# Kernel tuning notes

Hardware: AMD Instinct MI355X
Metric: run time of the kernel (lower is better)

The kernel has to match this reference:

```python
import jax, jax.numpy as jnp
import numpy as np

N = 8192          # number of nodes
IN_F = 256        # in_features
OUT_F = 128       # out_features
ALPHA = 0.2       # LeakyReLU negative slope


def setup_inputs() -> dict:
    key = jax.random.key(0)
    k1, k2, k3, k4 = jax.random.split(key, 4)
    h = jax.random.normal(k1, (N, IN_F), dtype=jnp.float32)
    adj = jax.random.randint(k2, (N, N), 0, 2, dtype=jnp.int32)  # dense 0/1 adjacency mask
    W = (jax.random.normal(k3, (IN_F, OUT_F), dtype=jnp.float32) * 0.05)   # W.weight^T
    a = (jax.random.normal(k4, (2 * OUT_F,), dtype=jnp.float32) * 0.05)    # a.weight flattened
    return {"h": h, "adj": adj, "W": W, "a": a}


def reference(h, adj, W, a):
    # Wh = self.W(h): [N, OUT_F]
    Wh = h @ W
    # Original builds an [N, N, 2F] concat tensor then projects with 'a'.
    # Equivalent math: e[i, j] = leaky_relu(Wh[i]@a1 + Wh[j]@a2)
    a1, a2 = a[:OUT_F], a[OUT_F:]
    src = Wh @ a1                                     # [N] per-source score
    dst = Wh @ a2                                     # [N] per-target score
    e = jax.nn.leaky_relu(src[:, None] + dst[None, :], negative_slope=ALPHA)  # [N, N]
    # masked softmax over neighbors (dim=1); adj==0 -> -inf
    e = jnp.where(adj == 0, -jnp.inf, e)
    attention = jax.nn.softmax(e, axis=1)             # [N, N]
    # dropout p=0 in eval-mode reference -> identity
    h_prime = attention @ Wh                          # [N, OUT_F]
    return jax.nn.elu(h_prime)                        # concat=True -> ELU
```

## Files before the change

### kernel.cpp

```cpp
#include <hip/hip_runtime.h>
#include <math.h>

#define N 8192
#define IN_F 256
#define OUT_F 128
#define ALPHA 0.2f

typedef _Float16 f16;
typedef __attribute__((ext_vector_type(4))) float f32x4;
typedef __attribute__((ext_vector_type(8))) _Float16 f16x8;
typedef __attribute__((ext_vector_type(4))) _Float16 f16x4;

__global__ __launch_bounds__(256) void k_prep(const float* __restrict__ W,
                                              f16* __restrict__ WT) {
    int idx = blockIdx.x * 256 + threadIdx.x;
    int f = idx >> 8;
    int k = idx & 255;
    WT[idx] = (f16)W[k * OUT_F + f];
}

#define HS 280
__global__ __launch_bounds__(256) void k_wh(const float* __restrict__ h,
                                            const f16* __restrict__ WT,
                                            const float* __restrict__ a,
                                            f16* __restrict__ WhT,
                                            float* __restrict__ src,
                                            float* __restrict__ dst) {
    __shared__ __align__(16) f16 hA[32][HS];
    __shared__ __align__(16) f16 outT[128][40];
    __shared__ float sred[4][32], dred[4][32];

    const int t = threadIdx.x;
    const int i0 = blockIdx.x * 32;
    const int wv = t >> 6, l = t & 63, ln = l & 15, lq = l >> 4;

    {
        const float4* hg = (const float4*)(h + (size_t)i0 * IN_F);
#pragma unroll
        for (int it = 0; it < 8; ++it) {
            int idx = t + it * 256;
            int r = idx >> 6;
            int c4 = (idx & 63) * 4;
            float4 v = hg[idx];
            f16x4 p = { (f16)v.x, (f16)v.y, (f16)v.z, (f16)v.w };
            *(f16x4*)&hA[r][c4] = p;
        }
    }
    __syncthreads();

    f32x4 acc00 = {0.f,0.f,0.f,0.f}, acc01 = {0.f,0.f,0.f,0.f};
    f32x4 acc10 = {0.f,0.f,0.f,0.f}, acc11 = {0.f,0.f,0.f,0.f};
    const int f0 = 32 * wv;

#pragma unroll
    for (int ks = 0; ks < 8; ++ks) {
        const int k0 = 32 * ks + 8 * lq;
        f16x8 a0 = *(const f16x8*)&hA[ln][k0];
        f16x8 a1 = *(const f16x8*)&hA[16 + ln][k0];
        f16x8 b0 = *(const f16x8*)(WT + (size_t)(f0 + ln) * IN_F + k0);
        f16x8 b1 = *(const f16x8*)(WT + (size_t)(f0 + 16 + ln) * IN_F + k0);
        acc00 = __builtin_amdgcn_mfma_f32_16x16x32_f16(a0, b0, acc00, 0, 0, 0);
        acc01 = __builtin_amdgcn_mfma_f32_16x16x32_f16(a0, b1, acc01, 0, 0, 0);
        acc10 = __builtin_amdgcn_mfma_f32_16x16x32_f16(a1, b0, acc10, 0, 0, 0);
        acc11 = __builtin_amdgcn_mfma_f32_16x16x32_f16(a1, b1, acc11, 0, 0, 0);
    }

    const float a1c0 = a[f0 + ln],      a2c0 = a[128 + f0 + ln];
    const float a1c1 = a[f0 + 16 + ln], a2c1 = a[128 + f0 + 16 + ln];
    float sp[8], dp[8];
#pragma unroll
    for (int i = 0; i < 8; ++i) { sp[i] = 0.f; dp[i] = 0.f; }

#pragma unroll
    for (int hh = 0; hh < 2; ++hh) {
        f32x4 v0 = hh ? acc10 : acc00;
        f32x4 v1 = hh ? acc11 : acc01;
        f16x4 p0, p1;
#pragma unroll
        for (int rg = 0; rg < 4; ++rg) {
            sp[hh * 4 + rg] += v0[rg] * a1c0 + v1[rg] * a1c1;
            dp[hh * 4 + rg] += v0[rg] * a2c0 + v1[rg] * a2c1;
            p0[rg] = (f16)v0[rg];
            p1[rg] = (f16)v1[rg];
        }
        *(f16x4*)&outT[f0 + ln][16 * hh + 4 * lq] = p0;
        *(f16x4*)&outT[f0 + 16 + ln][16 * hh + 4 * lq] = p1;
    }
#pragma unroll
    for (int i = 0; i < 8; ++i) {
        float s = sp[i], d = dp[i];
        s += __shfl_down(s, 8, 16); d += __shfl_down(d, 8, 16);
        s += __shfl_down(s, 4, 16); d += __shfl_down(d, 4, 16);
        s += __shfl_down(s, 2, 16); d += __shfl_down(d, 2, 16);
        s += __shfl_down(s, 1, 16); d += __shfl_down(d, 1, 16);
        if (ln == 0) {
            int row = 16 * (i >> 2) + 4 * lq + (i & 3);
            sred[wv][row] = s;
            dred[wv][row] = d;
        }
    }
    __syncthreads();
    if (t < 32) {
        src[i0 + t] = sred[0][t] + sred[1][t] + sred[2][t] + sred[3][t];
        dst[i0 + t] = dred[0][t] + dred[1][t] + dred[2][t] + dred[3][t];
    }
    {
        const int col = t & 127, g = t >> 7;
        const int ct = i0 >> 7, jo = i0 & 127;
        f16x8 q0 = *(const f16x8*)&outT[col][16 * g];
        f16x8 q1 = *(const f16x8*)&outT[col][16 * g + 8];
        f16* dstp = WhT + (size_t)ct * (128 * 128) + (size_t)col * 128 + jo + 16 * g;
        *(f16x8*)(dstp) = q0;
        *(f16x8*)(dstp + 8) = q1;
    }
}

#define TI 16
#define NJ 128
#define JS 2
#define NCL (N / NJ / JS)
#define WSTRIDE 152
__global__ __launch_bounds__(256, 4) void k_attn(const int* __restrict__ adj,
                                                 const f16* __restrict__ WhT,
                                                 const float* __restrict__ src,
                                                 const float* __restrict__ dst,
                                                 float* __restrict__ p_part,
                                                 float* __restrict__ l_part) {
    __shared__ __align__(16) f16 wA[2][TI][WSTRIDE];
    __shared__ float lfin[TI];

    const int t = threadIdx.x;
    const int i0 = blockIdx.x * TI;
    const int jh = blockIdx.y;
    const int pr = t >> 4;
    const int pm = t & 15;
    const int wv = t >> 6;
    const int l = t & 63, ln = l & 15, lq = l >> 4;

    const float my_src = src[i0 + pr];
    const float cshift = fabsf(my_src) + 4.0f;
    float lp = 0.f;
    f32x4 accv0 = {0.f,0.f,0.f,0.f}, accv1 = {0.f,0.f,0.f,0.f};

    const int* arow = adj + (size_t)(i0 + pr) * N + jh * (N / JS) + 8 * pm;
    const float* drow = dst + jh * (N / JS) + 8 * pm;
    const f16* Bb = WhT + (size_t)(jh * NCL) * (128 * 128)
                  + (size_t)(32 * wv + ln) * 128 + 8 * lq;

    int4 aA0, aB0, aA1, aB1;
    float4 dA0, dB0, dA1, dB1;

    auto issue = [&](int c, int4& xA, int4& xB, float4& xdA, float4& xdB) {
        const int j0 = c * NJ;
        xA = *(const int4*)(arow + j0);
        xB = *(const int4*)(arow + j0 + 4);
        xdA = *(const float4*)(drow + j0);
        xdB = *(const float4*)(drow + j0 + 4);
    };
    auto produce = [&](int c, const int4& xA, const int4& xB,
                       const float4& xdA, const float4& xdB) {
        float w[8];
        const int*   av = (const int*)&xA;
        const int*   bv = (const int*)&xB;
        const float* df = (const float*)&xdA;
        const float* ef = (const float*)&xdB;
#pragma unroll
        for (int k = 0; k < 4; ++k) {
            float e = my_src + df[k];
            float lk = e > 0.f ? e : ALPHA * e;
            w[k] = av[k] ? __expf(lk - cshift) : 0.f;
        }
#pragma unroll
        for (int k = 0; k < 4; ++k) {
            float e = my_src + ef[k];
            float lk = e > 0.f ? e : ALPHA * e;
            w[4 + k] = bv[k] ? __expf(lk - cshift) : 0.f;
        }
        f16x8 wp;
#pragma unroll
        for (int k = 0; k < 8; ++k) { lp += w[k]; wp[k] = (f16)w[k]; }
        *(f16x8*)&wA[c & 1][pr][8 * pm] = wp;
    };
    auto mpass = [&](int c) {
        const f16* wb = &wA[c & 1][0][0];
        const f16* bp = Bb + (size_t)c * (128 * 128);
#pragma unroll
        for (int ks = 0; ks < 4; ++ks) {
            const int k0 = 32 * ks;
            f16x8 a0 = *(const f16x8*)(wb + ln * WSTRIDE + k0 + 8 * lq);
            f16x8 b0 = *(const f16x8*)(bp + k0);
            f16x8 b1 = *(const f16x8*)(bp + 16 * 128 + k0);
            accv0 = __builtin_amdgcn_mfma_f32_16x16x32_f16(a0, b0, accv0, 0, 0, 0);
            accv1 = __builtin_amdgcn_mfma_f32_16x16x32_f16(a0, b1, accv1, 0, 0, 0);
        }
    };

    issue(0, aA0, aB0, dA0, dB0);
    produce(0, aA0, aB0, dA0, dB0);
    issue(1, aA1, aB1, dA1, dB1);
    __syncthreads();

    for (int cc = 0; cc < NCL; cc += 2) {
        if (cc + 2 < NCL) issue(cc + 2, aA0, aB0, dA0, dB0);
        mpass(cc);
        produce(cc + 1, aA1, aB1, dA1, dB1);
        __syncthreads();
        if (cc + 3 < NCL) issue(cc + 3, aA1, aB1, dA1, dB1);
        mpass(cc + 1);
        if (cc + 2 < NCL) produce(cc + 2, aA0, aB0, dA0, dB0);
        __syncthreads();
    }

    {
        float v = lp;
        v += __shfl_down(v, 8, 16);
        v += __shfl_down(v, 4, 16);
        v += __shfl_down(v, 2, 16);
        v += __shfl_down(v, 1, 16);
        if (pm == 0) lfin[pr] = v;
    }
    __syncthreads();
    if (t < TI) l_part[(size_t)jh * N + i0 + t] = lfin[t];

    float* pb = p_part + (size_t)jh * N * OUT_F;
#pragma unroll
    for (int hh = 0; hh < 2; ++hh) {
        f32x4 av = hh ? accv1 : accv0;
#pragma unroll
        for (int rg = 0; rg < 4; ++rg) {
            const int row = 4 * lq + rg;
            pb[(size_t)(i0 + row) * OUT_F + 32 * wv + 16 * hh + ln] = av[rg];
        }
    }
}

__global__ __launch_bounds__(256) void k_comb(const float* __restrict__ p_part,
                                              const float* __restrict__ l_part,
                                              float* __restrict__ out) {
    const int idx = blockIdx.x * 256 + threadIdx.x;
    const int row = idx >> 7;
    float p = p_part[idx] + p_part[(size_t)N * OUT_F + idx];
    float lsum = l_part[row] + l_part[N + row];
    float hp = p / lsum;
    out[idx] = hp > 0.f ? hp : expm1f(hp);
}

extern "C" void kernel_launch(void* const* d_in, const int* in_sizes, int n_in,
                              void* d_out, int out_size, void* d_ws, size_t ws_size,
                              hipStream_t stream) {
    const float* h   = (const float*)d_in[0];
    const int*   adj = (const int*)d_in[1];
    const float* W   = (const float*)d_in[2];
    const float* a   = (const float*)d_in[3];
    float* out = (float*)d_out;

    char* ws = (char*)d_ws;
    f16*   WT     = (f16*)ws;                       ws += 64 * 1024;
    f16*   WhT    = (f16*)ws;                       ws += 2 * 1024 * 1024;
    float* src    = (float*)ws;                     ws += N * sizeof(float);
    float* dst    = (float*)ws;                     ws += N * sizeof(float);
    float* l_part = (float*)ws;                     ws += JS * N * sizeof(float);
    float* p_part = (float*)ws;

    k_prep<<<128, 256, 0, stream>>>(W, WT);
    k_wh<<<N / 32, 256, 0, stream>>>(h, WT, a, WhT, src, dst);
    dim3 agrid(N / TI, JS);
    k_attn<<<agrid, 256, 0, stream>>>(adj, WhT, src, dst, p_part, l_part);
    k_comb<<<N * OUT_F / 256, 256, 0, stream>>>(p_part, l_part, out);
}
```

Measured before the change: 450.1 us.

## Restructure attention kernel: per-wave 32-row tiles with register-resident weights, 8-way j split

```diff
diff --git a/kernel.cpp b/kernel.cpp
--- a/kernel.cpp
+++ b/kernel.cpp
@@ -5,6 +5,8 @@
 #define IN_F 256
 #define OUT_F 128
 #define ALPHA 0.2f
+#define JS 8
+#define NSTEP 32
 
 typedef _Float16 f16;
 typedef __attribute__((ext_vector_type(4))) float f32x4;
@@ -115,121 +117,110 @@
     }
 }
 
-#define TI 16
-#define NJ 128
-#define JS 2
-#define NCL (N / NJ / JS)
-#define WSTRIDE 152
-__global__ __launch_bounds__(256, 4) void k_attn(const int* __restrict__ adj,
+__global__ __launch_bounds__(256, 2) void k_attn(const int* __restrict__ adj,
                                                  const f16* __restrict__ WhT,
                                                  const float* __restrict__ src,
                                                  const float* __restrict__ dst,
                                                  float* __restrict__ p_part,
                                                  float* __restrict__ l_part) {
-    __shared__ __align__(16) f16 wA[2][TI][WSTRIDE];
-    __shared__ float lfin[TI];
-
     const int t = threadIdx.x;
-    const int i0 = blockIdx.x * TI;
-    const int jh = blockIdx.y;
-    const int pr = t >> 4;
-    const int pm = t & 15;
-    const int wv = t >> 6;
-    const int l = t & 63, ln = l & 15, lq = l >> 4;
-
-    const float my_src = src[i0 + pr];
-    const float cshift = fabsf(my_src) + 4.0f;
-    float lp = 0.f;
-    f32x4 accv0 = {0.f,0.f,0.f,0.f}, accv1 = {0.f,0.f,0.f,0.f};
-
-    const int* arow = adj + (size_t)(i0 + pr) * N + jh * (N / JS) + 8 * pm;
-    const float* drow = dst + jh * (N / JS) + 8 * pm;
-    const f16* Bb = WhT + (size_t)(jh * NCL) * (128 * 128)
-                  + (size_t)(32 * wv + ln) * 128 + 8 * lq;
-
-    int4 aA0, aB0, aA1, aB1;
-    float4 dA0, dB0, dA1, dB1;
-
-    auto issue = [&](int c, int4& xA, int4& xB, float4& xdA, float4& xdB) {
-        const int j0 = c * NJ;
-        xA = *(const int4*)(arow + j0);
-        xB = *(const int4*)(arow + j0 + 4);
-        xdA = *(const float4*)(drow + j0);
-        xdB = *(const float4*)(drow + j0 + 4);
+    const int wv = t >> 6, l = t & 63, ln = l & 15, lq = l >> 4;
+    const int i0 = (blockIdx.x * 4 + wv) * 32;
+    const int jq = blockIdx.y;
+    const int jbase = jq * (N / JS);
+
+    const float src0 = src[i0 + ln];
+    const float src1 = src[i0 + 16 + ln];
+    const float c0 = fabsf(src0) + 4.0f;
+    const float c1 = fabsf(src1) + 4.0f;
+    float lp0 = 0.f, lp1 = 0.f;
+
+    f32x4 acc0[8], acc1[8];
+#pragma unroll
+    for (int ft = 0; ft < 8; ++ft) {
+        acc0[ft] = (f32x4){0.f,0.f,0.f,0.f};
+        acc1[ft] = (f32x4){0.f,0.f,0.f,0.f};
+    }
+
+    const int* arow0 = adj + (size_t)(i0 + ln) * N + jbase + 8 * lq;
+    const int* arow1 = arow0 + (size_t)16 * N;
+    const float* drow = dst + jbase + 8 * lq;
+    const f16* Bb = WhT + (size_t)(jq * 8) * (128 * 128) + (size_t)ln * 128 + 8 * lq;
+
+    int4 pa0[2][2], pa1[2][2];
+    float4 pd[2][2];
+
+    auto issue = [&](int s, int p) {
+        const int off = 32 * (s & (NSTEP - 1));
+        pa0[p][0] = *(const int4*)(arow0 + off);
+        pa0[p][1] = *(const int4*)(arow0 + off + 4);
+        pa1[p][0] = *(const int4*)(arow1 + off);
+        pa1[p][1] = *(const int4*)(arow1 + off + 4);
+        pd[p][0]  = *(const float4*)(drow + off);
+        pd[p][1]  = *(const float4*)(drow + off + 4);
     };
-    auto produce = [&](int c, const int4& xA, const int4& xB,
-                       const float4& xdA, const float4& xdB) {
-        float w[8];
-        const int*   av = (const int*)&xA;
-        const int*   bv = (const int*)&xB;
-        const float* df = (const float*)&xdA;
-        const float* ef = (const float*)&xdB;
+
+    issue(0, 0);
+    issue(1, 1);
+
+#pragma unroll 4
+    for (int s = 0; s < NSTEP; ++s) {
+        const int p = s & 1;
+        const int4 a00 = pa0[p][0], a01 = pa0[p][1];
+        const int4 a10 = pa1[p][0], a11 = pa1[p][1];
+        const float4 d0 = pd[p][0], d1 = pd[p][1];
+        issue(s + 2, p);
+
+        const int* av0 = (const int*)&a00;
+        const int* av1 = (const int*)&a01;
+        const int* bv0 = (const int*)&a10;
+        const int* bv1 = (const int*)&a11;
+        const float* df0 = (const float*)&d0;
+        const float* df1 = (const float*)&d1;
+
+        f16x8 af0, af1;
 #pragma unroll
         for (int k = 0; k < 4; ++k) {
-            float e = my_src + df[k];
-            float lk = e > 0.f ? e : ALPHA * e;
-            w[k] = av[k] ? __expf(lk - cshift) : 0.f;
+            float e0 = src0 + df0[k];
+            float w0 = av0[k] ? __expf(fmaxf(e0, ALPHA * e0) - c0) : 0.f;
+            lp0 += w0; af0[k] = (f16)w0;
+            float e1 = src1 + df0[k];
+            float w1 = bv0[k] ? __expf(fmaxf(e1, ALPHA * e1) - c1) : 0.f;
+            lp1 += w1; af1[k] = (f16)w1;
         }
 #pragma unroll
         for (int k = 0; k < 4; ++k) {
-            float e = my_src + ef[k];
-            float lk = e > 0.f ? e : ALPHA * e;
-            w[4 + k] = bv[k] ? __expf(lk - cshift) : 0.f;
-        }
-        f16x8 wp;
-#pragma unroll
-        for (int k = 0; k < 8; ++k) { lp += w[k]; wp[k] = (f16)w[k]; }
-        *(f16x8*)&wA[c & 1][pr][8 * pm] = wp;
-    };
-    auto mpass = [&](int c) {
-        const f16* wb = &wA[c & 1][0][0];
-        const f16* bp = Bb + (size_t)c * (128 * 128);
-#pragma unroll
-        for (int ks = 0; ks < 4; ++ks) {
-            const int k0 = 32 * ks;
-            f16x8 a0 = *(const f16x8*)(wb + ln * WSTRIDE + k0 + 8 * lq);
-            f16x8 b0 = *(const f16x8*)(bp + k0);
-            f16x8 b1 = *(const f16x8*)(bp + 16 * 128 + k0);
-            accv0 = __builtin_amdgcn_mfma_f32_16x16x32_f16(a0, b0, accv0, 0, 0, 0);
-            accv1 = __builtin_amdgcn_mfma_f32_16x16x32_f16(a0, b1, accv1, 0, 0, 0);
-        }
-    };
-
-    issue(0, aA0, aB0, dA0, dB0);
-    produce(0, aA0, aB0, dA0, dB0);
-    issue(1, aA1, aB1, dA1, dB1);
-    __syncthreads();
-
-    for (int cc = 0; cc < NCL; cc += 2) {
-        if (cc + 2 < NCL) issue(cc + 2, aA0, aB0, dA0, dB0);
-        mpass(cc);
-        produce(cc + 1, aA1, aB1, dA1, dB1);
-        __syncthreads();
-        if (cc + 3 < NCL) issue(cc + 3, aA1, aB1, dA1, dB1);
-        mpass(cc + 1);
-        if (cc + 2 < NCL) produce(cc + 2, aA0, aB0, dA0, dB0);
-        __syncthreads();
-    }
-
-    {
-        float v = lp;
-        v += __shfl_down(v, 8, 16);
-        v += __shfl_down(v, 4, 16);
-        v += __shfl_down(v, 2, 16);
-        v += __shfl_down(v, 1, 16);
-        if (pm == 0) lfin[pr] = v;
-    }
-    __syncthreads();
-    if (t < TI) l_part[(size_t)jh * N + i0 + t] = lfin[t];
-
-    float* pb = p_part + (size_t)jh * N * OUT_F;
-#pragma unroll
-    for (int hh = 0; hh < 2; ++hh) {
-        f32x4 av = hh ? accv1 : accv0;
+            float e0 = src0 + df1[k];
+            float w0 = av1[k] ? __expf(fmaxf(e0, ALPHA * e0) - c0) : 0.f;
+            lp0 += w0; af0[4 + k] = (f16)w0;
+            float e1 = src1 + df1[k];
+            float w1 = bv1[k] ? __expf(fmaxf(e1, ALPHA * e1) - c1) : 0.f;
+            lp1 += w1; af1[4 + k] = (f16)w1;
+        }
+
+        const f16* bp = Bb + (s >> 2) * (128 * 128) + (s & 3) * 32;
+#pragma unroll
+        for (int ft = 0; ft < 8; ++ft) {
+            f16x8 bf = *(const f16x8*)(bp + ft * (16 * 128));
+            acc0[ft] = __builtin_amdgcn_mfma_f32_16x16x32_f16(af0, bf, acc0[ft], 0, 0, 0);
+            acc1[ft] = __builtin_amdgcn_mfma_f32_16x16x32_f16(af1, bf, acc1[ft], 0, 0, 0);
+        }
+    }
+
+    lp0 += __shfl_down(lp0, 32); lp0 += __shfl_down(lp0, 16);
+    lp1 += __shfl_down(lp1, 32); lp1 += __shfl_down(lp1, 16);
+    if (l < 16) {
+        l_part[(size_t)jq * N + i0 + l] = lp0;
+        l_part[(size_t)jq * N + i0 + 16 + l] = lp1;
+    }
+
+    float* pb = p_part + (size_t)jq * N * OUT_F;
+#pragma unroll
+    for (int ft = 0; ft < 8; ++ft) {
 #pragma unroll
         for (int rg = 0; rg < 4; ++rg) {
-            const int row = 4 * lq + rg;
-            pb[(size_t)(i0 + row) * OUT_F + 32 * wv + 16 * hh + ln] = av[rg];
+            pb[(size_t)(i0 + 4 * lq + rg) * OUT_F + 16 * ft + ln] = acc0[ft][rg];
+            pb[(size_t)(i0 + 16 + 4 * lq + rg) * OUT_F + 16 * ft + ln] = acc1[ft][rg];
         }
     }
 }
@@ -237,12 +228,24 @@
 __global__ __launch_bounds__(256) void k_comb(const float* __restrict__ p_part,
                                               const float* __restrict__ l_part,
                                               float* __restrict__ out) {
-    const int idx = blockIdx.x * 256 + threadIdx.x;
-    const int row = idx >> 7;
-    float p = p_part[idx] + p_part[(size_t)N * OUT_F + idx];
-    float lsum = l_part[row] + l_part[N + row];
-    float hp = p / lsum;
-    out[idx] = hp > 0.f ? hp : expm1f(hp);
+    const int idx4 = blockIdx.x * 256 + threadIdx.x;
+    const int row = idx4 >> 5;
+    const float4* pp = (const float4*)p_part;
+    float4 p = pp[idx4];
+    float lsum = l_part[row];
+#pragma unroll
+    for (int q = 1; q < JS; ++q) {
+        float4 v = pp[(size_t)q * (N * OUT_F / 4) + idx4];
+        p.x += v.x; p.y += v.y; p.z += v.z; p.w += v.w;
+        lsum += l_part[(size_t)q * N + row];
+    }
+    float inv = 1.0f / lsum;
+    float4 r;
+    r.x = p.x * inv; r.x = r.x > 0.f ? r.x : expm1f(r.x);
+    r.y = p.y * inv; r.y = r.y > 0.f ? r.y : expm1f(r.y);
+    r.z = p.z * inv; r.z = r.z > 0.f ? r.z : expm1f(r.z);
+    r.w = p.w * inv; r.w = r.w > 0.f ? r.w : expm1f(r.w);
+    ((float4*)out)[idx4] = r;
 }
 
 extern "C" void kernel_launch(void* const* d_in, const int* in_sizes, int n_in,
@@ -259,12 +262,12 @@
     f16*   WhT    = (f16*)ws;                       ws += 2 * 1024 * 1024;
     float* src    = (float*)ws;                     ws += N * sizeof(float);
     float* dst    = (float*)ws;                     ws += N * sizeof(float);
-    float* l_part = (float*)ws;                     ws += JS * N * sizeof(float);
+    float* l_part = (float*)ws;                     ws += (size_t)JS * N * sizeof(float);
     float* p_part = (float*)ws;
 
     k_prep<<<128, 256, 0, stream>>>(W, WT);
     k_wh<<<N / 32, 256, 0, stream>>>(h, WT, a, WhT, src, dst);
-    dim3 agrid(N / TI, JS);
+    dim3 agrid(N / 128, JS);
     k_attn<<<agrid, 256, 0, stream>>>(adj, WhT, src, dst, p_part, l_part);
-    k_comb<<<N * OUT_F / 256, 256, 0, stream>>>(p_part, l_part, out);
-}
+    k_comb<<<N * OUT_F / 4 / 256, 256, 0, stream>>>(p_part, l_part, out);
+}
```

Measured after the change: 443.4 us. Within noise of the previous version (-1.5%).
